# Optimization experiments

Measured on AMD Instinct MI355X. Metric: run time of the kernel, lower is better.

## Reference

```python
import jax, jax.numpy as jnp
import numpy as np

D_MODEL = 512
N_HEADS = 8
D_HEAD = D_MODEL // N_HEADS


def setup_inputs() -> dict:
    key = jax.random.key(0)
    ks = jax.random.split(key, 10)
    B, N = 4, 2048
    s = 1.0 / np.sqrt(D_MODEL)
    inp = {
        'x': jax.random.normal(ks[0], (B, N, D_MODEL), jnp.float32),
        'attn_bias': jax.random.normal(ks[1], (B, 1, N, N), jnp.float32),
        'wq': jax.random.normal(ks[2], (D_MODEL, D_MODEL), jnp.float32) * s,
        'bq': jnp.zeros((D_MODEL,), jnp.float32),
        'wk': jax.random.normal(ks[3], (D_MODEL, D_MODEL), jnp.float32) * s,
        'bk': jnp.zeros((D_MODEL,), jnp.float32),
        'wv': jax.random.normal(ks[4], (D_MODEL, D_MODEL), jnp.float32) * s,
        'bv': jnp.zeros((D_MODEL,), jnp.float32),
        'wo': jax.random.normal(ks[5], (D_MODEL, D_MODEL), jnp.float32) * s,
        'bo': jnp.zeros((D_MODEL,), jnp.float32),
    }
    return inp


def reference(x, attn_bias, wq, bq, wk, bk, wv, bv, wo, bo):
    B, N, D = x.shape
    h, dh = N_HEADS, D_HEAD
    # projections; weights stored as (in, out) so y = x @ w + b
    q = (x @ wq + bq).reshape(B, N, h, dh).transpose(0, 2, 1, 3)  # (B,h,N,dh)
    k = (x @ wk + bk).reshape(B, N, h, dh).transpose(0, 2, 1, 3)
    v = (x @ wv + bv).reshape(B, N, h, dh).transpose(0, 2, 1, 3)
    scores = jnp.einsum('bhnd,bhmd->bhnm', q, k) / jnp.sqrt(jnp.float32(dh))
    scores = scores + attn_bias  # broadcast over heads
    attn = jax.nn.softmax(scores, axis=-1)
    out = jnp.einsum('bhnm,bhmd->bhnd', attn, v)
    out = out.transpose(0, 2, 1, 3).reshape(B, N, D)
    return out @ wo + bo
```

## Files before the change

### kernel.cpp

```cpp
#include <hip/hip_runtime.h>
#include <hip/hip_bf16.h>

typedef __bf16 bf16x8 __attribute__((ext_vector_type(8)));
typedef float f32x4 __attribute__((ext_vector_type(4)));
typedef float f32x16 __attribute__((ext_vector_type(16)));
using u16 = unsigned short;
using u32 = unsigned int;

#define LDSS 72

__device__ __forceinline__ u16 f2bf(float f) {
  union { float f; u32 u; } v; v.f = f;
  u32 r = v.u + 0x7fffu + ((v.u >> 16) & 1u);
  return (u16)(r >> 16);
}

__device__ __forceinline__ u32 cvt_pk_bf16(float lo, float hi) {
  u32 r;
  asm("v_cvt_pk_bf16_f32 %0, %1, %2" : "=v"(r) : "v"(lo), "v"(hi));
  return r;
}

__global__ void cast_x_kernel(const float* __restrict__ x, u16* __restrict__ xb) {
  int i = (blockIdx.x * 256 + threadIdx.x) * 8;
  float4 f0 = *(const float4*)&x[i];
  float4 f1 = *(const float4*)&x[i + 4];
  u16 u[8];
  u[0] = f2bf(f0.x); u[1] = f2bf(f0.y); u[2] = f2bf(f0.z); u[3] = f2bf(f0.w);
  u[4] = f2bf(f1.x); u[5] = f2bf(f1.y); u[6] = f2bf(f1.z); u[7] = f2bf(f1.w);
  *(uint4*)&xb[i] = *(uint4*)u;
}

__global__ void cast_wT_kernel(const float* __restrict__ w0, const float* __restrict__ w1,
                               const float* __restrict__ w2, const float* __restrict__ w3,
                               u16* __restrict__ t0, u16* __restrict__ t1,
                               u16* __restrict__ t2, u16* __restrict__ t3) {
  int i = blockIdx.x * 256 + threadIdx.x;
  int wi = i >> 18;
  int r = i & 262143;
  int row = r >> 9, col = r & 511;
  const float* w; u16* t;
  if (wi == 0)      { w = w0; t = t0; }
  else if (wi == 1) { w = w1; t = t1; }
  else if (wi == 2) { w = w2; t = t2; }
  else              { w = w3; t = t3; }
  t[col * 512 + row] = f2bf(w[r]);
}

__global__ __launch_bounds__(256) void proj_kernel(
    const u16* __restrict__ xb,
    const u16* __restrict__ wqT, const u16* __restrict__ wkT, const u16* __restrict__ wvT,
    const float* __restrict__ bq, const float* __restrict__ bk, const float* __restrict__ bv,
    u16* __restrict__ Q, u16* __restrict__ K, u16* __restrict__ Vt) {
  __shared__ u16 Alds[64 * LDSS];
  __shared__ u16 Blds[64 * LDSS];
  int which = blockIdx.z;
  const u16* wT; const float* bias; u16* out;
  if (which == 0)      { wT = wqT; bias = bq; out = Q; }
  else if (which == 1) { wT = wkT; bias = bk; out = K; }
  else                 { wT = wvT; bias = bv; out = Vt; }

  int m0 = blockIdx.y * 64;
  int n0 = blockIdx.x * 64;
  int tid = threadIdx.x;
  int lane = tid & 63, w = tid >> 6;
  int wm = w >> 1, wn = w & 1;
  int l15 = lane & 15, l4 = lane >> 4;

  int r0 = tid >> 3, c8 = (tid & 7) * 8;

  uint4 ar0 = *(const uint4*)&xb[(m0 + r0) * 512 + c8];
  uint4 ar1 = *(const uint4*)&xb[(m0 + r0 + 32) * 512 + c8];
  uint4 br0 = *(const uint4*)&wT[(n0 + r0) * 512 + c8];
  uint4 br1 = *(const uint4*)&wT[(n0 + r0 + 32) * 512 + c8];

  f32x4 acc[2][2] = {};
  for (int ks = 0; ks < 8; ks++) {
    __syncthreads();
    *(uint4*)&Alds[r0 * LDSS + c8]        = ar0;
    *(uint4*)&Alds[(r0 + 32) * LDSS + c8] = ar1;
    *(uint4*)&Blds[r0 * LDSS + c8]        = br0;
    *(uint4*)&Blds[(r0 + 32) * LDSS + c8] = br1;
    __syncthreads();
    if (ks < 7) {
      int k0 = (ks + 1) * 64;
      ar0 = *(const uint4*)&xb[(m0 + r0) * 512 + k0 + c8];
      ar1 = *(const uint4*)&xb[(m0 + r0 + 32) * 512 + k0 + c8];
      br0 = *(const uint4*)&wT[(n0 + r0) * 512 + k0 + c8];
      br1 = *(const uint4*)&wT[(n0 + r0 + 32) * 512 + k0 + c8];
    }
#pragma unroll
    for (int kk = 0; kk < 2; kk++) {
      bf16x8 a[2], b[2];
#pragma unroll
      for (int f = 0; f < 2; f++) {
        a[f] = *(const bf16x8*)&Alds[(wm * 32 + f * 16 + l15) * LDSS + kk * 32 + l4 * 8];
        b[f] = *(const bf16x8*)&Blds[(wn * 32 + f * 16 + l15) * LDSS + kk * 32 + l4 * 8];
      }
#pragma unroll
      for (int fm = 0; fm < 2; fm++)
#pragma unroll
        for (int fn = 0; fn < 2; fn++) {
          if (which == 2)
            acc[fm][fn] = __builtin_amdgcn_mfma_f32_16x16x32_bf16(b[fn], a[fm], acc[fm][fn], 0, 0, 0);
          else
            acc[fm][fn] = __builtin_amdgcn_mfma_f32_16x16x32_bf16(a[fm], b[fn], acc[fm][fn], 0, 0, 0);
        }
    }
  }
  int bidx = m0 >> 11;
  int head = n0 >> 6;
  if (which == 2) {
#pragma unroll
    for (int fm = 0; fm < 2; fm++)
#pragma unroll
      for (int fn = 0; fn < 2; fn++)
#pragma unroll
        for (int r = 0; r < 4; r++) {
          int drow = wn * 32 + fn * 16 + l4 * 4 + r;
          int col  = wm * 32 + fm * 16 + l15;
          float vv = acc[fm][fn][r] + bias[n0 + drow];
          out[((size_t)(bidx * 8 + head) * 64 + drow) * 2048 + (m0 & 2047) + col] = f2bf(vv);
        }
  } else {
#pragma unroll
    for (int fm = 0; fm < 2; fm++)
#pragma unroll
      for (int fn = 0; fn < 2; fn++)
#pragma unroll
        for (int r = 0; r < 4; r++) {
          int row = wm * 32 + fm * 16 + l4 * 4 + r;
          int col = wn * 32 + fn * 16 + l15;
          int nrow = (m0 & 2047) + row;
          float vv = acc[fm][fn][r] + bias[n0 + col];
          out[(((size_t)(bidx * 8 + head) * 2048) + nrow) * 64 + col] = f2bf(vv);
        }
  }
}

__global__ __launch_bounds__(256, 2) void attn_kernel(
    const u16* __restrict__ Q, const u16* __restrict__ K, const u16* __restrict__ Vt,
    const float* __restrict__ bias, u16* __restrict__ O) {
  __shared__ u16 Klds[64 * LDSS];
  __shared__ u16 Vtlds[64 * LDSS];

  int qt = blockIdx.x, h = blockIdx.y, b = blockIdx.z;
  int tid = threadIdx.x;
  int lane = tid & 63, w = tid >> 6;
  int l31 = lane & 31, hi = lane >> 5;
  int qrow = qt * 128 + w * 32 + l31;

  const u16* Qbh  = Q  + (size_t)(b * 8 + h) * 2048 * 64;
  const u16* Kbh  = K  + (size_t)(b * 8 + h) * 2048 * 64;
  const u16* Vtbh = Vt + (size_t)(b * 8 + h) * 64 * 2048;
  const float* biasq = bias + (size_t)b * 2048 * 2048 + (size_t)qrow * 2048;

  bf16x8 qf[4];
#pragma unroll
  for (int dk = 0; dk < 4; dk++)
    qf[dk] = *(const bf16x8*)&Qbh[qrow * 64 + dk * 16 + hi * 8];

  f32x16 o[2] = {};
  float mrow = -1e30f, lrow = 0.f;

  int r0 = tid >> 3, c8 = (tid & 7) * 8;

  uint4 kr0 = *(const uint4*)&Kbh[r0 * 64 + c8];
  uint4 kr1 = *(const uint4*)&Kbh[(32 + r0) * 64 + c8];
  uint4 vr0 = *(const uint4*)&Vtbh[r0 * 2048 + c8];
  uint4 vr1 = *(const uint4*)&Vtbh[(r0 + 32) * 2048 + c8];
  float4 bb[8];
#pragma unroll
  for (int kt = 0; kt < 2; kt++)
#pragma unroll
    for (int g = 0; g < 4; g++)
      bb[kt * 4 + g] = *(const float4*)&biasq[kt * 32 + 8 * g + 4 * hi];

  for (int t = 0; t < 32; t++) {
    __syncthreads();
    *(uint4*)&Klds[r0 * LDSS + c8]         = kr0;
    *(uint4*)&Klds[(r0 + 32) * LDSS + c8]  = kr1;
    *(uint4*)&Vtlds[r0 * LDSS + c8]        = vr0;
    *(uint4*)&Vtlds[(r0 + 32) * LDSS + c8] = vr1;
    __syncthreads();

    bool pf = (t < 31);
    if (pf) {
      kr0 = *(const uint4*)&Kbh[((t + 1) * 64 + r0) * 64 + c8];
      kr1 = *(const uint4*)&Kbh[((t + 1) * 64 + 32 + r0) * 64 + c8];
      vr0 = *(const uint4*)&Vtbh[r0 * 2048 + (t + 1) * 64 + c8];
      vr1 = *(const uint4*)&Vtbh[(r0 + 32) * 2048 + (t + 1) * 64 + c8];
    }

    f32x16 s[2] = {};
    __builtin_amdgcn_s_setprio(1);
#pragma unroll
    for (int dk = 0; dk < 4; dk++) {
      bf16x8 a0 = *(const bf16x8*)&Klds[l31 * LDSS + dk * 16 + hi * 8];
      s[0] = __builtin_amdgcn_mfma_f32_32x32x16_bf16(a0, qf[dk], s[0], 0, 0, 0);
      bf16x8 a1 = *(const bf16x8*)&Klds[(32 + l31) * LDSS + dk * 16 + hi * 8];
      s[1] = __builtin_amdgcn_mfma_f32_32x32x16_bf16(a1, qf[dk], s[1], 0, 0, 0);
    }
    __builtin_amdgcn_s_setprio(0);

    float m = -1e30f;
#pragma unroll
    for (int kt = 0; kt < 2; kt++)
#pragma unroll
      for (int g = 0; g < 4; g++) {
        float4 bv4 = bb[kt * 4 + g];
#pragma unroll
        for (int j = 0; j < 4; j++) {
          float val = s[kt][g * 4 + j] * 0.125f + ((const float*)&bv4)[j];
          s[kt][g * 4 + j] = val;
          m = fmaxf(m, val);
        }
      }
    m = fmaxf(m, __shfl_xor(m, 32));

    if (!__all(m <= mrow + 8.0f)) {
      float mnew = fmaxf(mrow, m);
      float corr = __expf(mrow - mnew);
      mrow = mnew;
      lrow *= corr;
#pragma unroll
      for (int dt = 0; dt < 2; dt++)
#pragma unroll
        for (int i = 0; i < 16; i++) o[dt][i] *= corr;
    }

    u32 c[2][8];
    float sum = 0.f;
#pragma unroll
    for (int kt = 0; kt < 2; kt++)
#pragma unroll
      for (int g = 0; g < 4; g++) {
        float p0 = __expf(s[kt][g * 4 + 0] - mrow);
        float p1 = __expf(s[kt][g * 4 + 1] - mrow);
        float p2 = __expf(s[kt][g * 4 + 2] - mrow);
        float p3 = __expf(s[kt][g * 4 + 3] - mrow);
        sum += (p0 + p1) + (p2 + p3);
        c[kt][2 * g]     = cvt_pk_bf16(p0, p1);
        c[kt][2 * g + 1] = cvt_pk_bf16(p2, p3);
      }
    sum += __shfl_xor(sum, 32);
    lrow += sum;

    u32 dx[2][8];
#pragma unroll
    for (int kt = 0; kt < 2; kt++)
#pragma unroll
      for (int j = 0; j < 8; j++)
        dx[kt][j] = (u32)__shfl_xor((int)c[kt][j], 32);

    if (pf) {
#pragma unroll
      for (int kt = 0; kt < 2; kt++)
#pragma unroll
        for (int g = 0; g < 4; g++)
          bb[kt * 4 + g] = *(const float4*)&biasq[(t + 1) * 64 + kt * 32 + 8 * g + 4 * hi];
    }

    __builtin_amdgcn_s_setprio(1);
#pragma unroll
    for (int kk = 0; kk < 4; kk++) {
      const int kt = kk >> 1, jA = 4 * (kk & 1);
      union { u32 u[4]; bf16x8 v; } pfg;
      pfg.u[0] = hi ? dx[kt][jA + 2] : c[kt][jA];
      pfg.u[1] = hi ? dx[kt][jA + 3] : c[kt][jA + 1];
      pfg.u[2] = hi ? c[kt][jA + 2]  : dx[kt][jA];
      pfg.u[3] = hi ? c[kt][jA + 3]  : dx[kt][jA + 1];
#pragma unroll
      for (int dt = 0; dt < 2; dt++) {
        bf16x8 va = *(const bf16x8*)&Vtlds[(dt * 32 + l31) * LDSS + kk * 16 + hi * 8];
        o[dt] = __builtin_amdgcn_mfma_f32_32x32x16_bf16(va, pfg.v, o[dt], 0, 0, 0);
      }
    }
    __builtin_amdgcn_s_setprio(0);
  }

  float inv = 1.0f / lrow;
  size_t obase = (size_t)(b * 2048 + qrow) * 512 + h * 64;
#pragma unroll
  for (int dt = 0; dt < 2; dt++)
#pragma unroll
    for (int g = 0; g < 4; g++) {
      uint2 pr;
      pr.x = cvt_pk_bf16(o[dt][4 * g + 0] * inv, o[dt][4 * g + 1] * inv);
      pr.y = cvt_pk_bf16(o[dt][4 * g + 2] * inv, o[dt][4 * g + 3] * inv);
      *(uint2*)&O[obase + dt * 32 + 8 * g + 4 * hi] = pr;
    }
}

__global__ __launch_bounds__(256) void outproj_kernel(
    const u16* __restrict__ Ob, const u16* __restrict__ woT,
    const float* __restrict__ bo, float* __restrict__ out) {
  __shared__ u16 Alds[64 * LDSS];
  __shared__ u16 Blds[64 * LDSS];
  int m0 = blockIdx.y * 64;
  int n0 = blockIdx.x * 64;
  int tid = threadIdx.x;
  int lane = tid & 63, w = tid >> 6;
  int wm = w >> 1, wn = w & 1;
  int l15 = lane & 15, l4 = lane >> 4;

  int r0 = tid >> 3, c8 = (tid & 7) * 8;
  uint4 ar0 = *(const uint4*)&Ob[(m0 + r0) * 512 + c8];
  uint4 ar1 = *(const uint4*)&Ob[(m0 + r0 + 32) * 512 + c8];
  uint4 br0 = *(const uint4*)&woT[(n0 + r0) * 512 + c8];
  uint4 br1 = *(const uint4*)&woT[(n0 + r0 + 32) * 512 + c8];

  f32x4 acc[2][2] = {};
  for (int ks = 0; ks < 8; ks++) {
    __syncthreads();
    *(uint4*)&Alds[r0 * LDSS + c8]        = ar0;
    *(uint4*)&Alds[(r0 + 32) * LDSS + c8] = ar1;
    *(uint4*)&Blds[r0 * LDSS + c8]        = br0;
    *(uint4*)&Blds[(r0 + 32) * LDSS + c8] = br1;
    __syncthreads();
    if (ks < 7) {
      int k0 = (ks + 1) * 64;
      ar0 = *(const uint4*)&Ob[(m0 + r0) * 512 + k0 + c8];
      ar1 = *(const uint4*)&Ob[(m0 + r0 + 32) * 512 + k0 + c8];
      br0 = *(const uint4*)&woT[(n0 + r0) * 512 + k0 + c8];
      br1 = *(const uint4*)&woT[(n0 + r0 + 32) * 512 + k0 + c8];
    }
#pragma unroll
    for (int kk = 0; kk < 2; kk++) {
      bf16x8 a[2], bfr[2];
#pragma unroll
      for (int f = 0; f < 2; f++) {
        a[f] = *(const bf16x8*)&Alds[(wm * 32 + f * 16 + l15) * LDSS + kk * 32 + l4 * 8];
        bfr[f] = *(const bf16x8*)&Blds[(wn * 32 + f * 16 + l15) * LDSS + kk * 32 + l4 * 8];
      }
#pragma unroll
      for (int fm = 0; fm < 2; fm++)
#pragma unroll
        for (int fn = 0; fn < 2; fn++)
          acc[fm][fn] = __builtin_amdgcn_mfma_f32_16x16x32_bf16(a[fm], bfr[fn], acc[fm][fn], 0, 0, 0);
    }
  }
#pragma unroll
  for (int fm = 0; fm < 2; fm++)
#pragma unroll
    for (int fn = 0; fn < 2; fn++)
#pragma unroll
      for (int r = 0; r < 4; r++) {
        int row = wm * 32 + fm * 16 + l4 * 4 + r;
        int col = wn * 32 + fn * 16 + l15;
        out[(size_t)(m0 + row) * 512 + n0 + col] = acc[fm][fn][r] + bo[n0 + col];
      }
}

extern "C" void kernel_launch(void* const* d_in, const int* in_sizes, int n_in,
                              void* d_out, int out_size, void* d_ws, size_t ws_size,
                              hipStream_t stream) {
  const float* x    = (const float*)d_in[0];
  const float* bias = (const float*)d_in[1];
  const float* wq   = (const float*)d_in[2];
  const float* bq   = (const float*)d_in[3];
  const float* wk   = (const float*)d_in[4];
  const float* bk   = (const float*)d_in[5];
  const float* wv   = (const float*)d_in[6];
  const float* bv   = (const float*)d_in[7];
  const float* wo   = (const float*)d_in[8];
  const float* bo   = (const float*)d_in[9];
  float* out = (float*)d_out;

  char* ws = (char*)d_ws;
  u16* xb  = (u16*)(ws + 0);
  u16* wqT = (u16*)(ws + 8388608);
  u16* wkT = (u16*)(ws + 8912896);
  u16* wvT = (u16*)(ws + 9437184);
  u16* woT = (u16*)(ws + 9961472);
  u16* Qb  = (u16*)(ws + 10485760);
  u16* Kb  = (u16*)(ws + 18874368);
  u16* VtB = (u16*)(ws + 27262976);
  u16* Ob  = (u16*)(ws + 35651584);

  hipLaunchKernelGGL(cast_x_kernel, dim3(2048), dim3(256), 0, stream, x, xb);
  hipLaunchKernelGGL(cast_wT_kernel, dim3(4096), dim3(256), 0, stream,
                     wq, wk, wv, wo, wqT, wkT, wvT, woT);
  hipLaunchKernelGGL(proj_kernel, dim3(8, 128, 3), dim3(256), 0, stream,
                     xb, wqT, wkT, wvT, bq, bk, bv, Qb, Kb, VtB);
  hipLaunchKernelGGL(attn_kernel, dim3(16, 8, 4), dim3(256), 0, stream,
                     Qb, Kb, VtB, bias, Ob);
  hipLaunchKernelGGL(outproj_kernel, dim3(8, 128), dim3(256), 0, stream,
                     Ob, woT, bo, out);
}
```

Before: 139.8 us.

## Split attention key range across two wave groups and merge partial softmax

The attention block doubles to 512 threads, and two groups of four waves each process half of the key tiles (split-KV inside a block) with separate LDS buffers. The partial outputs and the running max and sum from the second group are merged through LDS using log-sum-exp rescaling before the store. The change also reorders the bias and K/V prefetch, loading the second half of the bias late, and moves the lane-swap shuffles into the PV loop to lower register pressure. It aims to raise the number of waves in flight to hide latency, at the cost of extra LDS traffic, a merge step and more barriers.

New measurement: 148.2 us. 6.1% more time.

```diff
diff --git a/kernel.cpp b/kernel.cpp
--- a/kernel.cpp
+++ b/kernel.cpp
@@ -8,6 +8,7 @@
 using u32 = unsigned int;
 
 #define LDSS 72
+#define TILE (64 * LDSS)
 
 __device__ __forceinline__ u16 f2bf(float f) {
   union { float f; u32 u; } v; v.f = f;
@@ -138,23 +139,27 @@
   }
 }
 
-__global__ __launch_bounds__(256, 2) void attn_kernel(
+__global__ __launch_bounds__(512, 2) void attn_kernel(
     const u16* __restrict__ Q, const u16* __restrict__ K, const u16* __restrict__ Vt,
     const float* __restrict__ bias, u16* __restrict__ O) {
-  __shared__ u16 Klds[64 * LDSS];
-  __shared__ u16 Vtlds[64 * LDSS];
+  __shared__ u16 smem[4 * TILE];
 
   int qt = blockIdx.x, h = blockIdx.y, b = blockIdx.z;
   int tid = threadIdx.x;
   int lane = tid & 63, w = tid >> 6;
+  int g2 = w >> 2, ww = w & 3;
   int l31 = lane & 31, hi = lane >> 5;
-  int qrow = qt * 128 + w * 32 + l31;
+  int qrow = qt * 128 + ww * 32 + l31;
 
   const u16* Qbh  = Q  + (size_t)(b * 8 + h) * 2048 * 64;
   const u16* Kbh  = K  + (size_t)(b * 8 + h) * 2048 * 64;
   const u16* Vtbh = Vt + (size_t)(b * 8 + h) * 64 * 2048;
   const float* biasq = bias + (size_t)b * 2048 * 2048 + (size_t)qrow * 2048;
 
+  u16* Kl = smem + g2 * TILE;
+  u16* Vl = smem + (2 + g2) * TILE;
+  const int tbase = g2 * 16;
+
   bf16x8 qf[4];
 #pragma unroll
   for (int dk = 0; dk < 4; dk++)
@@ -163,59 +168,71 @@
   f32x16 o[2] = {};
   float mrow = -1e30f, lrow = 0.f;
 
-  int r0 = tid >> 3, c8 = (tid & 7) * 8;
-
-  uint4 kr0 = *(const uint4*)&Kbh[r0 * 64 + c8];
-  uint4 kr1 = *(const uint4*)&Kbh[(32 + r0) * 64 + c8];
-  uint4 vr0 = *(const uint4*)&Vtbh[r0 * 2048 + c8];
-  uint4 vr1 = *(const uint4*)&Vtbh[(r0 + 32) * 2048 + c8];
-  float4 bb[8];
-#pragma unroll
-  for (int kt = 0; kt < 2; kt++)
-#pragma unroll
-    for (int g = 0; g < 4; g++)
-      bb[kt * 4 + g] = *(const float4*)&biasq[kt * 32 + 8 * g + 4 * hi];
-
-  for (int t = 0; t < 32; t++) {
-    __syncthreads();
-    *(uint4*)&Klds[r0 * LDSS + c8]         = kr0;
-    *(uint4*)&Klds[(r0 + 32) * LDSS + c8]  = kr1;
-    *(uint4*)&Vtlds[r0 * LDSS + c8]        = vr0;
-    *(uint4*)&Vtlds[(r0 + 32) * LDSS + c8] = vr1;
-    __syncthreads();
-
-    bool pf = (t < 31);
-    if (pf) {
-      kr0 = *(const uint4*)&Kbh[((t + 1) * 64 + r0) * 64 + c8];
-      kr1 = *(const uint4*)&Kbh[((t + 1) * 64 + 32 + r0) * 64 + c8];
-      vr0 = *(const uint4*)&Vtbh[r0 * 2048 + (t + 1) * 64 + c8];
-      vr1 = *(const uint4*)&Vtbh[(r0 + 32) * 2048 + (t + 1) * 64 + c8];
-    }
+  int tid2 = tid & 255;
+  int r0 = tid2 >> 3, c8 = (tid2 & 7) * 8;
+
+  uint4 kr0 = *(const uint4*)&Kbh[(tbase * 64 + r0) * 64 + c8];
+  uint4 kr1 = *(const uint4*)&Kbh[(tbase * 64 + r0 + 32) * 64 + c8];
+  uint4 vr0 = *(const uint4*)&Vtbh[r0 * 2048 + tbase * 64 + c8];
+  uint4 vr1 = *(const uint4*)&Vtbh[(r0 + 32) * 2048 + tbase * 64 + c8];
+  float4 bb0[4];
+#pragma unroll
+  for (int g = 0; g < 4; g++)
+    bb0[g] = *(const float4*)&biasq[tbase * 64 + 8 * g + 4 * hi];
+
+  for (int t = 0; t < 16; t++) {
+    __syncthreads();
+    *(uint4*)&Kl[r0 * LDSS + c8]        = kr0;
+    *(uint4*)&Kl[(r0 + 32) * LDSS + c8] = kr1;
+    *(uint4*)&Vl[r0 * LDSS + c8]        = vr0;
+    *(uint4*)&Vl[(r0 + 32) * LDSS + c8] = vr1;
+    __syncthreads();
+
+    int tile = tbase + t;
+    bool pf = (t < 15);
 
     f32x16 s[2] = {};
     __builtin_amdgcn_s_setprio(1);
 #pragma unroll
     for (int dk = 0; dk < 4; dk++) {
-      bf16x8 a0 = *(const bf16x8*)&Klds[l31 * LDSS + dk * 16 + hi * 8];
+      bf16x8 a0 = *(const bf16x8*)&Kl[l31 * LDSS + dk * 16 + hi * 8];
       s[0] = __builtin_amdgcn_mfma_f32_32x32x16_bf16(a0, qf[dk], s[0], 0, 0, 0);
-      bf16x8 a1 = *(const bf16x8*)&Klds[(32 + l31) * LDSS + dk * 16 + hi * 8];
+      bf16x8 a1 = *(const bf16x8*)&Kl[(32 + l31) * LDSS + dk * 16 + hi * 8];
       s[1] = __builtin_amdgcn_mfma_f32_32x32x16_bf16(a1, qf[dk], s[1], 0, 0, 0);
     }
     __builtin_amdgcn_s_setprio(0);
 
-    float m = -1e30f;
-#pragma unroll
-    for (int kt = 0; kt < 2; kt++)
-#pragma unroll
-      for (int g = 0; g < 4; g++) {
-        float4 bv4 = bb[kt * 4 + g];
-#pragma unroll
-        for (int j = 0; j < 4; j++) {
-          float val = s[kt][g * 4 + j] * 0.125f + ((const float*)&bv4)[j];
-          s[kt][g * 4 + j] = val;
-          m = fmaxf(m, val);
-        }
-      }
+    float4 b1[4];
+#pragma unroll
+    for (int g = 0; g < 4; g++)
+      b1[g] = *(const float4*)&biasq[tile * 64 + 32 + 8 * g + 4 * hi];
+
+    float mx[8];
+#pragma unroll
+    for (int g = 0; g < 4; g++) {
+      float4 bv4 = bb0[g];
+      float v0 = s[0][g * 4 + 0] * 0.125f + bv4.x;
+      float v1 = s[0][g * 4 + 1] * 0.125f + bv4.y;
+      float v2 = s[0][g * 4 + 2] * 0.125f + bv4.z;
+      float v3 = s[0][g * 4 + 3] * 0.125f + bv4.w;
+      s[0][g * 4 + 0] = v0; s[0][g * 4 + 1] = v1;
+      s[0][g * 4 + 2] = v2; s[0][g * 4 + 3] = v3;
+      mx[g] = fmaxf(fmaxf(v0, v1), fmaxf(v2, v3));
+    }
+#pragma unroll
+    for (int g = 0; g < 4; g++) {
+      float4 bv4 = b1[g];
+      float v0 = s[1][g * 4 + 0] * 0.125f + bv4.x;
+      float v1 = s[1][g * 4 + 1] * 0.125f + bv4.y;
+      float v2 = s[1][g * 4 + 2] * 0.125f + bv4.z;
+      float v3 = s[1][g * 4 + 3] * 0.125f + bv4.w;
+      s[1][g * 4 + 0] = v0; s[1][g * 4 + 1] = v1;
+      s[1][g * 4 + 2] = v2; s[1][g * 4 + 3] = v3;
+      mx[4 + g] = fmaxf(fmaxf(v0, v1), fmaxf(v2, v3));
+    }
+    mx[0] = fmaxf(mx[0], mx[4]); mx[1] = fmaxf(mx[1], mx[5]);
+    mx[2] = fmaxf(mx[2], mx[6]); mx[3] = fmaxf(mx[3], mx[7]);
+    float m = fmaxf(fmaxf(mx[0], mx[1]), fmaxf(mx[2], mx[3]));
     m = fmaxf(m, __shfl_xor(m, 32));
 
     if (!__all(m <= mrow + 8.0f)) {
@@ -230,7 +247,7 @@
     }
 
     u32 c[2][8];
-    float sum = 0.f;
+    float sm[8];
 #pragma unroll
     for (int kt = 0; kt < 2; kt++)
 #pragma unroll
@@ -239,57 +256,82 @@
         float p1 = __expf(s[kt][g * 4 + 1] - mrow);
         float p2 = __expf(s[kt][g * 4 + 2] - mrow);
         float p3 = __expf(s[kt][g * 4 + 3] - mrow);
-        sum += (p0 + p1) + (p2 + p3);
+        sm[kt * 4 + g] = (p0 + p1) + (p2 + p3);
         c[kt][2 * g]     = cvt_pk_bf16(p0, p1);
         c[kt][2 * g + 1] = cvt_pk_bf16(p2, p3);
       }
+    sm[0] += sm[4]; sm[1] += sm[5]; sm[2] += sm[6]; sm[3] += sm[7];
+    float sum = (sm[0] + sm[1]) + (sm[2] + sm[3]);
     sum += __shfl_xor(sum, 32);
     lrow += sum;
 
-    u32 dx[2][8];
-#pragma unroll
-    for (int kt = 0; kt < 2; kt++)
-#pragma unroll
-      for (int j = 0; j < 8; j++)
-        dx[kt][j] = (u32)__shfl_xor((int)c[kt][j], 32);
-
     if (pf) {
-#pragma unroll
-      for (int kt = 0; kt < 2; kt++)
-#pragma unroll
-        for (int g = 0; g < 4; g++)
-          bb[kt * 4 + g] = *(const float4*)&biasq[(t + 1) * 64 + kt * 32 + 8 * g + 4 * hi];
+      int kb = (tile + 1) * 64;
+      kr0 = *(const uint4*)&Kbh[(kb + r0) * 64 + c8];
+      kr1 = *(const uint4*)&Kbh[(kb + r0 + 32) * 64 + c8];
+      vr0 = *(const uint4*)&Vtbh[r0 * 2048 + kb + c8];
+      vr1 = *(const uint4*)&Vtbh[(r0 + 32) * 2048 + kb + c8];
+#pragma unroll
+      for (int g = 0; g < 4; g++)
+        bb0[g] = *(const float4*)&biasq[kb + 8 * g + 4 * hi];
     }
 
     __builtin_amdgcn_s_setprio(1);
 #pragma unroll
     for (int kk = 0; kk < 4; kk++) {
       const int kt = kk >> 1, jA = 4 * (kk & 1);
+      u32 d0 = (u32)__shfl_xor((int)c[kt][jA + 0], 32);
+      u32 d1 = (u32)__shfl_xor((int)c[kt][jA + 1], 32);
+      u32 d2 = (u32)__shfl_xor((int)c[kt][jA + 2], 32);
+      u32 d3 = (u32)__shfl_xor((int)c[kt][jA + 3], 32);
       union { u32 u[4]; bf16x8 v; } pfg;
-      pfg.u[0] = hi ? dx[kt][jA + 2] : c[kt][jA];
-      pfg.u[1] = hi ? dx[kt][jA + 3] : c[kt][jA + 1];
-      pfg.u[2] = hi ? c[kt][jA + 2]  : dx[kt][jA];
-      pfg.u[3] = hi ? c[kt][jA + 3]  : dx[kt][jA + 1];
+      pfg.u[0] = hi ? d2 : c[kt][jA + 0];
+      pfg.u[1] = hi ? d3 : c[kt][jA + 1];
+      pfg.u[2] = hi ? c[kt][jA + 2] : d0;
+      pfg.u[3] = hi ? c[kt][jA + 3] : d1;
 #pragma unroll
       for (int dt = 0; dt < 2; dt++) {
-        bf16x8 va = *(const bf16x8*)&Vtlds[(dt * 32 + l31) * LDSS + kk * 16 + hi * 8];
+        bf16x8 va = *(const bf16x8*)&Vl[(dt * 32 + l31) * LDSS + kk * 16 + hi * 8];
         o[dt] = __builtin_amdgcn_mfma_f32_32x32x16_bf16(va, pfg.v, o[dt], 0, 0, 0);
       }
     }
     __builtin_amdgcn_s_setprio(0);
   }
 
-  float inv = 1.0f / lrow;
-  size_t obase = (size_t)(b * 2048 + qrow) * 512 + h * 64;
-#pragma unroll
-  for (int dt = 0; dt < 2; dt++)
-#pragma unroll
-    for (int g = 0; g < 4; g++) {
-      uint2 pr;
-      pr.x = cvt_pk_bf16(o[dt][4 * g + 0] * inv, o[dt][4 * g + 1] * inv);
-      pr.y = cvt_pk_bf16(o[dt][4 * g + 2] * inv, o[dt][4 * g + 3] * inv);
-      *(uint2*)&O[obase + dt * 32 + 8 * g + 4 * hi] = pr;
-    }
+  __syncthreads();
+  float* olds = (float*)smem;
+  float2* mllds = (float2*)(smem + (4 * 32 * 64) * 2);
+
+  if (g2 == 1) {
+    mllds[ww * 64 + lane] = make_float2(mrow, lrow);
+#pragma unroll
+    for (int dt = 0; dt < 2; dt++)
+#pragma unroll
+      for (int i = 0; i < 16; i++)
+        olds[(ww * 32 + dt * 16 + i) * 64 + lane] = o[dt][i];
+  }
+  __syncthreads();
+  if (g2 == 0) {
+    float2 ml = mllds[ww * 64 + lane];
+    float M = fmaxf(mrow, ml.x);
+    float w0 = __expf(mrow - M), w1 = __expf(ml.x - M);
+    float linv = 1.0f / (lrow * w0 + ml.y * w1);
+    float cw0 = w0 * linv, cw1 = w1 * linv;
+    size_t obase = (size_t)(b * 2048 + qrow) * 512 + h * 64;
+#pragma unroll
+    for (int dt = 0; dt < 2; dt++)
+#pragma unroll
+      for (int g = 0; g < 4; g++) {
+        float v0 = o[dt][4 * g + 0] * cw0 + olds[(ww * 32 + dt * 16 + 4 * g + 0) * 64 + lane] * cw1;
+        float v1 = o[dt][4 * g + 1] * cw0 + olds[(ww * 32 + dt * 16 + 4 * g + 1) * 64 + lane] * cw1;
+        float v2 = o[dt][4 * g + 2] * cw0 + olds[(ww * 32 + dt * 16 + 4 * g + 2) * 64 + lane] * cw1;
+        float v3 = o[dt][4 * g + 3] * cw0 + olds[(ww * 32 + dt * 16 + 4 * g + 3) * 64 + lane] * cw1;
+        uint2 pr;
+        pr.x = cvt_pk_bf16(v0, v1);
+        pr.y = cvt_pk_bf16(v2, v3);
+        *(uint2*)&O[obase + dt * 32 + 8 * g + 4 * hi] = pr;
+      }
+  }
 }
 
 __global__ __launch_bounds__(256) void outproj_kernel(
@@ -383,7 +425,7 @@
                      wq, wk, wv, wo, wqT, wkT, wvT, woT);
   hipLaunchKernelGGL(proj_kernel, dim3(8, 128, 3), dim3(256), 0, stream,
                      xb, wqT, wkT, wvT, bq, bk, bv, Qb, Kb, VtB);
-  hipLaunchKernelGGL(attn_kernel, dim3(16, 8, 4), dim3(256), 0, stream,
+  hipLaunchKernelGGL(attn_kernel, dim3(16, 8, 4), dim3(512), 0, stream,
                      Qb, Kb, VtB, bias, Ob);
   hipLaunchKernelGGL(outproj_kernel, dim3(8, 128), dim3(256), 0, stream,
                      Ob, woT, bo, out);
```
